# Optimization experiments

Hardware: AMD Instinct MI355X
Metric: run time of the kernel (lower is better)

## Reference

```python
import jax, jax.numpy as jnp
import numpy as np

DS = 16
NUM_INPUTS = 13
WIDTH = 64
DEPTH = 5
NUM_OUTPUTS = 3
# channels of the per-pixel MLP: input gets 4*log2(ds) cosine coord channels
CH = [NUM_INPUTS + 4 * int(np.log2(DS))] + [WIDTH] * (DEPTH - 1) + [NUM_OUTPUTS]


def _splits():
    biases, weights, idx = [], [], 0
    for l in range(len(CH) - 1):
        nci, nco = CH[l], CH[l + 1]
        biases.append((idx, idx + nco)); idx += nco
        weights.append((idx, idx + nco * nci)); idx += nco * nci
    return biases, weights, idx

BIAS_SPLITS, WEIGHT_SPLITS, NUM_PARAMS = _splits()


def _get_coords(bs, h, w, ds):
    """Cosine positional encoding, 4 channels per octave of ds."""
    two_pi = 2.0 * np.pi
    chans = []
    f = ds
    x = jnp.arange(w, dtype=jnp.float32)
    y = jnp.arange(h, dtype=jnp.float32)
    while f > 1:
        px = two_pi * jnp.remainder(x, f) / f  # [w]
        py = two_pi * jnp.remainder(y, f) / f  # [h]
        xcos = jnp.broadcast_to(jnp.cos(px)[None, None, None, :], (bs, 1, h, w))
        xsin = jnp.broadcast_to(jnp.sin(px)[None, None, None, :], (bs, 1, h, w))
        ycos = jnp.broadcast_to(jnp.cos(py)[None, None, :, None], (bs, 1, h, w))
        ysin = jnp.broadcast_to(jnp.sin(py)[None, None, :, None], (bs, 1, h, w))
        chans += [xcos, xsin, ycos, ysin]
        f //= 2
    return jnp.concatenate(chans, axis=1)  # [bs, 4*log2(ds), h, w]


def setup_inputs() -> dict:
    key = jax.random.key(0)
    k1, k2 = jax.random.split(key)
    bs, h, w = 4, 512, 512
    h_lr, w_lr = h // DS, w // DS
    highres = jax.random.normal(k1, (bs, NUM_INPUTS, h, w), dtype=jnp.float32)
    lr_params = jax.random.normal(k2, (bs, NUM_PARAMS, h_lr, w_lr), dtype=jnp.float32)
    return {"highres": highres, "lr_params": lr_params}


def reference(highres, lr_params):
    k = DS
    bs, _, h, w = highres.shape
    _, _, h_lr, w_lr = lr_params.shape

    coords = _get_coords(bs, h, w, k)
    x = jnp.concatenate([highres, coords], axis=1)  # [bs, nci0, h, w]
    nci0 = x.shape[1]

    # unfold into k*k tiles per low-res pixel: [bs, h_lr, w_lr, k*k, nci0]
    tiles = (x.reshape(bs, nci0, h_lr, k, w_lr, k)
              .transpose(0, 2, 4, 3, 5, 1)
              .reshape(bs, h_lr, w_lr, k * k, nci0))

    out = tiles
    n_layers = len(CH) - 1
    for l in range(n_layers):
        nci, nco = CH[l], CH[l + 1]
        ws, we = WEIGHT_SPLITS[l]
        b0, b1 = BIAS_SPLITS[l]
        w_ = (lr_params[:, ws:we].transpose(0, 2, 3, 1)
              .reshape(bs, h_lr, w_lr, nci, nco))
        b_ = (lr_params[:, b0:b1].transpose(0, 2, 3, 1)
              .reshape(bs, h_lr, w_lr, 1, nco))
        out = jnp.einsum('bhwpi,bhwio->bhwpo', out, w_) + b_
        if l < n_layers - 1:
            out = jnp.where(out >= 0, out, 0.01 * out)  # leaky_relu(0.01)
        else:
            out = jnp.tanh(out)

    # fold tiles back to [bs, num_outputs, h, w]
    out = (out.reshape(bs, h_lr, w_lr, k, k, NUM_OUTPUTS)
            .transpose(0, 5, 1, 3, 2, 4)
            .reshape(bs, NUM_OUTPUTS, h, w))
    return out
```

## Files before the change

kernel.cpp:

```cpp
#include <hip/hip_runtime.h>
#include <math.h>

#define NCH   14595
#define WROW  14596
#define HR_C  13
#define IMG_H 512
#define IMG_W 512
#define BS    4


__global__ __launch_bounds__(256) void transpose_params(const float* __restrict__ lp,
                                                        float* __restrict__ wsT) {
    __shared__ float tile[64][65];
    int bid = blockIdx.x;
    int pt = bid & 15;
    int t  = bid >> 4;
    int ct = t % 229;
    int b  = t / 229;
    int c0 = ct * 64, p0 = pt * 64;
    int tp = threadIdx.x & 63;
    int tr = threadIdx.x >> 6;
#pragma unroll
    for (int s = 0; s < 16; s++) {
        int c = c0 + tr + s * 4;
        if (c < NCH)
            tile[tr + s * 4][tp] = lp[((size_t)b * NCH + c) * 1024 + p0 + tp];
    }
    __syncthreads();
#pragma unroll
    for (int s = 0; s < 16; s++) {
        int p = p0 + tr + s * 4;
        int c = c0 + tp;
        if (c < NCH)
            wsT[((size_t)b * 1024 + p) * WROW + c] = tile[tp][tr + s * 4];
    }
}

__device__ __forceinline__ void block_sync_lds() {
    __builtin_amdgcn_sched_barrier(0);
    asm volatile("s_waitcnt lgkmcnt(0)" ::: "memory");
    __builtin_amdgcn_s_barrier();
    __builtin_amdgcn_sched_barrier(0);
}

template<int NCI, bool USE_WS>
__device__ __forceinline__ void mlp_layer(const float* __restrict__ actT,
                                          const float* __restrict__ wrow,
                                          const float* __restrict__ lp_col,
                                          int loff,
                                          int px0, int o0, float acc[4][8]) {
    if (USE_WS) {
        float4 b0 = *(const float4*)&wrow[o0];
        float4 b1 = *(const float4*)&wrow[o0 + 4];
#pragma unroll
        for (int i = 0; i < 4; i++) {
            acc[i][0] = b0.x; acc[i][1] = b0.y; acc[i][2] = b0.z; acc[i][3] = b0.w;
            acc[i][4] = b1.x; acc[i][5] = b1.y; acc[i][6] = b1.z; acc[i][7] = b1.w;
        }
    } else {
#pragma unroll
        for (int j = 0; j < 8; j++) {
            float bv = lp_col[(size_t)(loff + o0 + j) << 10];
#pragma unroll
            for (int i = 0; i < 4; i++) acc[i][j] = bv;
        }
    }
#pragma unroll 4
    for (int k = 0; k < NCI; k++) {
        float4 a = *(const float4*)&actT[k * 128 + px0];
        float4 w0, w1;
        if (USE_WS) {
            w0 = *(const float4*)&wrow[64 + (k << 6) + o0];
            w1 = *(const float4*)&wrow[64 + (k << 6) + o0 + 4];
        } else {
            int e = loff + 64 + (k << 6) + o0;
            w0.x = lp_col[(size_t)(e + 0) << 10]; w0.y = lp_col[(size_t)(e + 1) << 10];
            w0.z = lp_col[(size_t)(e + 2) << 10]; w0.w = lp_col[(size_t)(e + 3) << 10];
            w1.x = lp_col[(size_t)(e + 4) << 10]; w1.y = lp_col[(size_t)(e + 5) << 10];
            w1.z = lp_col[(size_t)(e + 6) << 10]; w1.w = lp_col[(size_t)(e + 7) << 10];
        }
#pragma unroll
        for (int i = 0; i < 4; i++) {
            float av = (i == 0) ? a.x : (i == 1) ? a.y : (i == 2) ? a.z : a.w;
            acc[i][0] = fmaf(av, w0.x, acc[i][0]);
            acc[i][1] = fmaf(av, w0.y, acc[i][1]);
            acc[i][2] = fmaf(av, w0.z, acc[i][2]);
            acc[i][3] = fmaf(av, w0.w, acc[i][3]);
            acc[i][4] = fmaf(av, w1.x, acc[i][4]);
            acc[i][5] = fmaf(av, w1.y, acc[i][5]);
            acc[i][6] = fmaf(av, w1.z, acc[i][6]);
            acc[i][7] = fmaf(av, w1.w, acc[i][7]);
        }
    }
}

template<bool USE_WS>
__global__ __launch_bounds__(256, 4) void asap_main(const float* __restrict__ hr,
                                                    const float* __restrict__ lp,
                                                    const float* __restrict__ wsT,
                                                    float* __restrict__ out) {
    __shared__ __align__(16) float actT[64 * 128];

    int bid0 = blockIdx.x;
    int bid  = ((bid0 & 7) << 10) | (bid0 >> 3);

    int half = bid & 1;
    int x    = (bid >> 1) & 31;
    int y    = (bid >> 6) & 31;
    int b    = bid >> 11;
    int tid  = threadIdx.x;
    int pix  = y * 32 + x;

    const float* wrow   = wsT + ((size_t)b * 1024 + pix) * WROW;
    const float* lp_col = lp + (size_t)b * NCH * 1024 + pix;

    {
        int Y0 = y * 16 + half * 8, X0 = x * 16;
        for (int t = tid; t < HR_C * 128; t += 256) {
            int c = t >> 7, p = t & 127;
            int row = p >> 4, kx = p & 15;
            actT[c * 128 + p] =
                hr[(((size_t)b * HR_C + c) * IMG_H + Y0 + row) * IMG_W + X0 + kx];
        }
        if (tid < 128) {
            int p = tid, row = p >> 4, kx = p & 15;
            int kyg = half * 8 + row;
            const float two_pi = 6.28318530717958647692f;
            int f = 16;
#pragma unroll
            for (int fi = 0; fi < 4; fi++) {
                float ax = two_pi * (float)(kx & (f - 1)) / (float)f;
                float ay = two_pi * (float)(kyg & (f - 1)) / (float)f;
                actT[(13 + 4 * fi + 0) * 128 + p] = cosf(ax);
                actT[(13 + 4 * fi + 1) * 128 + p] = sinf(ax);
                actT[(13 + 4 * fi + 2) * 128 + p] = cosf(ay);
                actT[(13 + 4 * fi + 3) * 128 + p] = sinf(ay);
                f >>= 1;
            }
        }
    }
    block_sync_lds();

    int pg = tid & 31, og = tid >> 5;
    int px0 = pg << 2, o0 = og << 3;
    float acc[4][8];

    auto writeback = [&]() {
#pragma unroll
        for (int j = 0; j < 8; j++) {
            float4 v;
            v.x = acc[0][j]; v.y = acc[1][j]; v.z = acc[2][j]; v.w = acc[3][j];
            v.x = fmaxf(v.x, 0.01f * v.x);
            v.y = fmaxf(v.y, 0.01f * v.y);
            v.z = fmaxf(v.z, 0.01f * v.z);
            v.w = fmaxf(v.w, 0.01f * v.w);
            *(float4*)&actT[(o0 + j) * 128 + px0] = v;
        }
    };

    mlp_layer<29, USE_WS>(actT, wrow + 0,     lp_col, 0,     px0, o0, acc);
    block_sync_lds();
    writeback();
    block_sync_lds();

    mlp_layer<64, USE_WS>(actT, wrow + 1920,  lp_col, 1920,  px0, o0, acc);
    block_sync_lds();
    writeback();
    block_sync_lds();

    mlp_layer<64, USE_WS>(actT, wrow + 6080,  lp_col, 6080,  px0, o0, acc);
    block_sync_lds();
    writeback();
    block_sync_lds();

    mlp_layer<64, USE_WS>(actT, wrow + 10240, lp_col, 10240, px0, o0, acc);
    block_sync_lds();
    writeback();
    block_sync_lds();

    if (tid < 128) {
        int p = tid;
        float s0, s1, s2;
        if (USE_WS) {
            s0 = wrow[14400]; s1 = wrow[14401]; s2 = wrow[14402];
        } else {
            s0 = lp_col[(size_t)14400 << 10];
            s1 = lp_col[(size_t)14401 << 10];
            s2 = lp_col[(size_t)14402 << 10];
        }
#pragma unroll 4
        for (int k = 0; k < 64; k++) {
            float a = actT[k * 128 + p];
            float w0, w1, w2;
            if (USE_WS) {
                w0 = wrow[14403 + k * 3 + 0];
                w1 = wrow[14403 + k * 3 + 1];
                w2 = wrow[14403 + k * 3 + 2];
            } else {
                w0 = lp_col[(size_t)(14403 + k * 3 + 0) << 10];
                w1 = lp_col[(size_t)(14403 + k * 3 + 1) << 10];
                w2 = lp_col[(size_t)(14403 + k * 3 + 2) << 10];
            }
            s0 = fmaf(a, w0, s0);
            s1 = fmaf(a, w1, s1);
            s2 = fmaf(a, w2, s2);
        }
        int row = p >> 4, kx = p & 15;
        int Y = y * 16 + half * 8 + row, X = x * 16 + kx;
        size_t base = ((size_t)b * 3) * IMG_H * IMG_W + (size_t)Y * IMG_W + X;
        out[base]                             = tanhf(s0);
        out[base + (size_t)IMG_H * IMG_W]     = tanhf(s1);
        out[base + (size_t)2 * IMG_H * IMG_W] = tanhf(s2);
    }
}

extern "C" void kernel_launch(void* const* d_in, const int* in_sizes, int n_in,
                              void* d_out, int out_size, void* d_ws, size_t ws_size,
                              hipStream_t stream) {
    const float* hr = (const float*)d_in[0];
    const float* lp = (const float*)d_in[1];
    float* out = (float*)d_out;
    float* wsT = (float*)d_ws;

    size_t need = (size_t)BS * 1024 * WROW * sizeof(float);
    if (ws_size >= need) {
        transpose_params<<<BS * 229 * 16, 256, 0, stream>>>(lp, wsT);
        asap_main<true><<<8192, 256, 0, stream>>>(hr, lp, wsT, out);
    } else {
        asap_main<false><<<8192, 256, 0, stream>>>(hr, lp, wsT, out);
    }
}
```

Baseline: 637.3 us.

## Remap MLP threads so each wave owns 8 outputs with uniform weight loads

Switches the main kernel to 512 threads where each wave handles 8 output channels and each lane 2 pixels, making weight addresses wave-uniform so they can become scalar/broadcast 32-byte loads. Pads the transposed weight row stride to 14600 for alignment. The final 3-output layer is split across three waves with vectorized paired-pixel stores. This cuts per-thread register footprint and redundant vector weight loads, at the cost of less register reuse per activation load and higher LDS traffic per FMA.

Result: faster. 598.3 us (-6.1%).

```diff
diff --git a/kernel.cpp b/kernel.cpp
--- a/kernel.cpp
+++ b/kernel.cpp
@@ -2,11 +2,14 @@
 #include <math.h>
 
 #define NCH   14595
-#define WROW  14596
+#define WROW  14600
 #define HR_C  13
 #define IMG_H 512
 #define IMG_W 512
 #define BS    4
+
+typedef float f32x8 __attribute__((ext_vector_type(8)));
+typedef float f32x2 __attribute__((ext_vector_type(2)));
 
 
 __global__ __launch_bounds__(256) void transpose_params(const float* __restrict__ lp,
@@ -45,57 +48,38 @@
 
 template<int NCI, bool USE_WS>
 __device__ __forceinline__ void mlp_layer(const float* __restrict__ actT,
-                                          const float* __restrict__ wrow,
+                                          const float* __restrict__ wl,
                                           const float* __restrict__ lp_col,
-                                          int loff,
-                                          int px0, int o0, float acc[4][8]) {
-    if (USE_WS) {
-        float4 b0 = *(const float4*)&wrow[o0];
-        float4 b1 = *(const float4*)&wrow[o0 + 4];
-#pragma unroll
-        for (int i = 0; i < 4; i++) {
-            acc[i][0] = b0.x; acc[i][1] = b0.y; acc[i][2] = b0.z; acc[i][3] = b0.w;
-            acc[i][4] = b1.x; acc[i][5] = b1.y; acc[i][6] = b1.z; acc[i][7] = b1.w;
-        }
-    } else {
-#pragma unroll
-        for (int j = 0; j < 8; j++) {
-            float bv = lp_col[(size_t)(loff + o0 + j) << 10];
-#pragma unroll
-            for (int i = 0; i < 4; i++) acc[i][j] = bv;
-        }
+                                          int loff, int o0,
+                                          int px0, float acc[2][8]) {
+#pragma unroll
+    for (int j = 0; j < 8; j++) {
+        float bv = USE_WS ? wl[j] : lp_col[(size_t)(loff + o0 + j) << 10];
+        acc[0][j] = bv; acc[1][j] = bv;
     }
 #pragma unroll 4
     for (int k = 0; k < NCI; k++) {
-        float4 a = *(const float4*)&actT[k * 128 + px0];
-        float4 w0, w1;
+        f32x2 a = *(const f32x2*)&actT[k * 128 + px0];
         if (USE_WS) {
-            w0 = *(const float4*)&wrow[64 + (k << 6) + o0];
-            w1 = *(const float4*)&wrow[64 + (k << 6) + o0 + 4];
+            f32x8 w = *(const f32x8*)(wl + 64 + (k << 6));
+#pragma unroll
+            for (int j = 0; j < 8; j++) {
+                acc[0][j] = fmaf(a.x, w[j], acc[0][j]);
+                acc[1][j] = fmaf(a.y, w[j], acc[1][j]);
+            }
         } else {
-            int e = loff + 64 + (k << 6) + o0;
-            w0.x = lp_col[(size_t)(e + 0) << 10]; w0.y = lp_col[(size_t)(e + 1) << 10];
-            w0.z = lp_col[(size_t)(e + 2) << 10]; w0.w = lp_col[(size_t)(e + 3) << 10];
-            w1.x = lp_col[(size_t)(e + 4) << 10]; w1.y = lp_col[(size_t)(e + 5) << 10];
-            w1.z = lp_col[(size_t)(e + 6) << 10]; w1.w = lp_col[(size_t)(e + 7) << 10];
-        }
-#pragma unroll
-        for (int i = 0; i < 4; i++) {
-            float av = (i == 0) ? a.x : (i == 1) ? a.y : (i == 2) ? a.z : a.w;
-            acc[i][0] = fmaf(av, w0.x, acc[i][0]);
-            acc[i][1] = fmaf(av, w0.y, acc[i][1]);
-            acc[i][2] = fmaf(av, w0.z, acc[i][2]);
-            acc[i][3] = fmaf(av, w0.w, acc[i][3]);
-            acc[i][4] = fmaf(av, w1.x, acc[i][4]);
-            acc[i][5] = fmaf(av, w1.y, acc[i][5]);
-            acc[i][6] = fmaf(av, w1.z, acc[i][6]);
-            acc[i][7] = fmaf(av, w1.w, acc[i][7]);
+#pragma unroll
+            for (int j = 0; j < 8; j++) {
+                float w = lp_col[(size_t)(loff + 64 + (k << 6) + o0 + j) << 10];
+                acc[0][j] = fmaf(a.x, w, acc[0][j]);
+                acc[1][j] = fmaf(a.y, w, acc[1][j]);
+            }
         }
     }
 }
 
 template<bool USE_WS>
-__global__ __launch_bounds__(256, 4) void asap_main(const float* __restrict__ hr,
+__global__ __launch_bounds__(512, 8) void asap_main(const float* __restrict__ hr,
                                                     const float* __restrict__ lp,
                                                     const float* __restrict__ wsT,
                                                     float* __restrict__ out) {
@@ -109,6 +93,8 @@
     int y    = (bid >> 6) & 31;
     int b    = bid >> 11;
     int tid  = threadIdx.x;
+    int lane = tid & 63;
+    int wv   = __builtin_amdgcn_readfirstlane(tid >> 6);
     int pix  = y * 32 + x;
 
     const float* wrow   = wsT + ((size_t)b * 1024 + pix) * WROW;
@@ -116,7 +102,7 @@
 
     {
         int Y0 = y * 16 + half * 8, X0 = x * 16;
-        for (int t = tid; t < HR_C * 128; t += 256) {
+        for (int t = tid; t < HR_C * 128; t += 512) {
             int c = t >> 7, p = t & 127;
             int row = p >> 4, kx = p & 15;
             actT[c * 128 + p] =
@@ -141,76 +127,75 @@
     }
     block_sync_lds();
 
-    int pg = tid & 31, og = tid >> 5;
-    int px0 = pg << 2, o0 = og << 3;
-    float acc[4][8];
+    int o0  = wv << 3;
+    int px0 = lane << 1;
+    float acc[2][8];
 
     auto writeback = [&]() {
 #pragma unroll
         for (int j = 0; j < 8; j++) {
-            float4 v;
-            v.x = acc[0][j]; v.y = acc[1][j]; v.z = acc[2][j]; v.w = acc[3][j];
-            v.x = fmaxf(v.x, 0.01f * v.x);
-            v.y = fmaxf(v.y, 0.01f * v.y);
-            v.z = fmaxf(v.z, 0.01f * v.z);
-            v.w = fmaxf(v.w, 0.01f * v.w);
-            *(float4*)&actT[(o0 + j) * 128 + px0] = v;
+            f32x2 v;
+            v.x = fmaxf(acc[0][j], 0.01f * acc[0][j]);
+            v.y = fmaxf(acc[1][j], 0.01f * acc[1][j]);
+            *(f32x2*)&actT[(o0 + j) * 128 + px0] = v;
         }
     };
 
-    mlp_layer<29, USE_WS>(actT, wrow + 0,     lp_col, 0,     px0, o0, acc);
-    block_sync_lds();
-    writeback();
-    block_sync_lds();
-
-    mlp_layer<64, USE_WS>(actT, wrow + 1920,  lp_col, 1920,  px0, o0, acc);
-    block_sync_lds();
-    writeback();
-    block_sync_lds();
-
-    mlp_layer<64, USE_WS>(actT, wrow + 6080,  lp_col, 6080,  px0, o0, acc);
-    block_sync_lds();
-    writeback();
-    block_sync_lds();
-
-    mlp_layer<64, USE_WS>(actT, wrow + 10240, lp_col, 10240, px0, o0, acc);
-    block_sync_lds();
-    writeback();
-    block_sync_lds();
-
-    if (tid < 128) {
-        int p = tid;
-        float s0, s1, s2;
+    const float* wl0 = wrow + 0     + o0;
+    const float* wl1 = wrow + 1920  + o0;
+    const float* wl2 = wrow + 6080  + o0;
+    const float* wl3 = wrow + 10240 + o0;
+
+    mlp_layer<29, USE_WS>(actT, wl0, lp_col, 0,     o0, px0, acc);
+    block_sync_lds();
+    writeback();
+    block_sync_lds();
+
+    mlp_layer<64, USE_WS>(actT, wl1, lp_col, 1920,  o0, px0, acc);
+    block_sync_lds();
+    writeback();
+    block_sync_lds();
+
+    mlp_layer<64, USE_WS>(actT, wl2, lp_col, 6080,  o0, px0, acc);
+    block_sync_lds();
+    writeback();
+    block_sync_lds();
+
+    mlp_layer<64, USE_WS>(actT, wl3, lp_col, 10240, o0, px0, acc);
+    block_sync_lds();
+    writeback();
+    block_sync_lds();
+
+    if (wv < 3) {
+        float sA, sB;
         if (USE_WS) {
-            s0 = wrow[14400]; s1 = wrow[14401]; s2 = wrow[14402];
+            float bv = wrow[14400 + wv];
+            sA = bv; sB = bv;
+#pragma unroll 4
+            for (int k = 0; k < 64; k++) {
+                f32x2 a = *(const f32x2*)&actT[k * 128 + px0];
+                float w = wrow[14403 + k * 3 + wv];
+                sA = fmaf(a.x, w, sA);
+                sB = fmaf(a.y, w, sB);
+            }
         } else {
-            s0 = lp_col[(size_t)14400 << 10];
-            s1 = lp_col[(size_t)14401 << 10];
-            s2 = lp_col[(size_t)14402 << 10];
-        }
+            float bv = lp_col[(size_t)(14400 + wv) << 10];
+            sA = bv; sB = bv;
 #pragma unroll 4
-        for (int k = 0; k < 64; k++) {
-            float a = actT[k * 128 + p];
-            float w0, w1, w2;
-            if (USE_WS) {
-                w0 = wrow[14403 + k * 3 + 0];
-                w1 = wrow[14403 + k * 3 + 1];
-                w2 = wrow[14403 + k * 3 + 2];
-            } else {
-                w0 = lp_col[(size_t)(14403 + k * 3 + 0) << 10];
-                w1 = lp_col[(size_t)(14403 + k * 3 + 1) << 10];
-                w2 = lp_col[(size_t)(14403 + k * 3 + 2) << 10];
-            }
-            s0 = fmaf(a, w0, s0);
-            s1 = fmaf(a, w1, s1);
-            s2 = fmaf(a, w2, s2);
-        }
-        int row = p >> 4, kx = p & 15;
+            for (int k = 0; k < 64; k++) {
+                f32x2 a = *(const f32x2*)&actT[k * 128 + px0];
+                float w = lp_col[(size_t)(14403 + k * 3 + wv) << 10];
+                sA = fmaf(a.x, w, sA);
+                sB = fmaf(a.y, w, sB);
+            }
+        }
+        int row = px0 >> 4, kx = px0 & 15;
         int Y = y * 16 + half * 8 + row, X = x * 16 + kx;
-        size_t base = ((size_t)b * 3) * IMG_H * IMG_W + (size_t)Y * IMG_W + X;
-        out[base]                             = tanhf(s0);
-        out[base + (size_t)IMG_H * IMG_W]     = tanhf(s1);
-        out[base + (size_t)2 * IMG_H * IMG_W] = tanhf(s2);
+        size_t base = ((size_t)(b * 3 + wv)) * IMG_H * IMG_W + (size_t)Y * IMG_W + X;
+        f32x2 o;
+        o.x = tanhf(sA);
+        o.y = tanhf(sB);
+        *(f32x2*)&out[base] = o;
     }
 }
 
@@ -225,8 +210,8 @@
     size_t need = (size_t)BS * 1024 * WROW * sizeof(float);
     if (ws_size >= need) {
         transpose_params<<<BS * 229 * 16, 256, 0, stream>>>(lp, wsT);
-        asap_main<true><<<8192, 256, 0, stream>>>(hr, lp, wsT, out);
+        asap_main<true><<<8192, 512, 0, stream>>>(hr, lp, wsT, out);
     } else {
-        asap_main<false><<<8192, 256, 0, stream>>>(hr, lp, wsT, out);
-    }
-}
+        asap_main<false><<<8192, 512, 0, stream>>>(hr, lp, wsT, out);
+    }
+}
```
